# Kernel tuning notes

Measured on AMD Instinct MI355X. Metric: run time of the kernel, lower is better.

Reference implementation:

```python
import jax, jax.numpy as jnp
import numpy as np

N, E, D, H = 50000, 800000, 128, 8
DH = D // H  # 16
EPS_LN = 1e-5


def layer_norm(x, gamma, beta):
    mu = jnp.mean(x, axis=-1, keepdims=True)
    var = jnp.var(x, axis=-1, keepdims=True)
    return (x - mu) * jax.lax.rsqrt(var + EPS_LN) * gamma + beta


def setup_inputs() -> dict:
    key = jax.random.key(0)
    ks = jax.random.split(key, 12)
    s = 1.0 / np.sqrt(D)
    x = jax.random.normal(ks[0], (N, D), dtype=jnp.float32)
    src = jax.random.randint(ks[1], (E,), 0, N, dtype=jnp.int32)
    dst = jax.random.randint(ks[2], (E,), 0, N, dtype=jnp.int32)
    Wq = jax.random.normal(ks[3], (D, D), dtype=jnp.float32) * s
    Wk = jax.random.normal(ks[4], (D, D), dtype=jnp.float32) * s
    Wv = jax.random.normal(ks[5], (D, D), dtype=jnp.float32) * s
    Wo = jax.random.normal(ks[6], (D, D), dtype=jnp.float32) * s
    bq = jnp.zeros((D,), jnp.float32)
    bk = jnp.zeros((D,), jnp.float32)
    bv = jnp.zeros((D,), jnp.float32)
    bo = jnp.zeros((D,), jnp.float32)
    gamma1 = jnp.ones((D,), jnp.float32)
    beta1 = jnp.zeros((D,), jnp.float32)
    gamma2 = jnp.ones((D,), jnp.float32)
    beta2 = jnp.zeros((D,), jnp.float32)
    return dict(x=x, src=src, dst=dst, Wq=Wq, bq=bq, Wk=Wk, bk=bk, Wv=Wv, bv=bv,
                Wo=Wo, bo=bo, gamma1=gamma1, beta1=beta1, gamma2=gamma2, beta2=beta2)


def reference(x, src, dst, Wq, bq, Wk, bk, Wv, bv, Wo, bo, gamma1, beta1, gamma2, beta2):
    n = x.shape[0]
    Q = (x @ Wq + bq).reshape(n, H, DH)   # [N,H,Dh]
    K = (x @ Wk + bk).reshape(n, H, DH)
    V = (x @ Wv + bv).reshape(n, H, DH)
    # edge-wise QK dot: score[e,h] = sum_d K[src[e],h,d] * Q[dst[e],h,d]
    score = jnp.sum(K[src] * Q[dst], axis=-1) / np.sqrt(DH)  # [E,H]
    score = jnp.exp(jnp.clip(score, -5.0, 5.0))
    # scatter-sum weighted values and normalizer over destination nodes
    wV = jax.ops.segment_sum(V[src] * score[..., None], dst, num_segments=n)  # [N,H,Dh]
    z = jax.ops.segment_sum(score, dst, num_segments=n)                        # [N,H]
    attn = (wV / (z[..., None] + 1e-3)).reshape(n, D)
    h = layer_norm(x + attn, gamma1, beta1)
    # sublayer: h + relu(O(LN(h)))  (dropout = 0)
    h = h + jax.nn.relu(layer_norm(h, gamma2, beta2) @ Wo + bo)
    return h
```

## Files before the change

### kernel.cpp

```cpp
#include <hip/hip_runtime.h>

typedef unsigned short ushort_t;
typedef __attribute__((ext_vector_type(8))) short short8;
typedef __attribute__((ext_vector_type(4))) float floatx4;
typedef __attribute__((ext_vector_type(2))) _Float16 half2v;
typedef __attribute__((ext_vector_type(8))) _Float16 half8;

#define QSCALE 0.36067376022224085f
#define SCLIP  7.2134752044448170f

__device__ __forceinline__ unsigned h2u(half2v h) {
    union { half2v h; unsigned u; } x; x.h = h; return x.u;
}
__device__ __forceinline__ half2v u2h(unsigned u) {
    union { unsigned u; half2v h; } x; x.u = u; return x.h;
}
__device__ __forceinline__ ushort_t h2us(_Float16 h) {
    union { _Float16 h; ushort_t u; } x; x.h = h; return x.u;
}
__device__ __forceinline__ unsigned pkrtz(float a, float b) {
    auto h = __builtin_amdgcn_cvt_pkrtz(a, b);
    union { decltype(h) h2; unsigned u; } x; x.h2 = h; return x.u;
}
__device__ __forceinline__ float dot2h(half2v a, half2v b, float c) {
#if __has_builtin(__builtin_amdgcn_fdot2)
    return __builtin_amdgcn_fdot2(a, b, c, false);
#else
    return c + (float)a[0] * (float)b[0] + (float)a[1] * (float)b[1];
#endif
}
__device__ __forceinline__ half2v pk_shfl_add(half2v a, int m) {
    unsigned o = (unsigned)__shfl_xor((int)h2u(a), m, 64);
    return a + u2h(o);
}

__global__ __launch_bounds__(256) void transpose_swz(
    const float* __restrict__ Wq, const float* __restrict__ Wk,
    const float* __restrict__ Wv, const float* __restrict__ Wo,
    ushort_t* __restrict__ out, int* __restrict__ deg, int N)
{
    int flat = (blockIdx.y * gridDim.x + blockIdx.x) * 256 + threadIdx.x;
    for (int i = flat; i < N; i += 8192) deg[i] = 0;

    const float* W = (blockIdx.y == 0) ? Wq : (blockIdx.y == 1) ? Wk :
                     (blockIdx.y == 2) ? Wv : Wo;
    ushort_t* T = out + (size_t)blockIdx.y * 128 * 128;
    int t = blockIdx.x * 256 + threadIdx.x;
    int kg = t >> 7;
    int n  = t & 127;
    int k0 = kg * 8;
    float w[8];
    #pragma unroll
    for (int j = 0; j < 8; j++)
        w[j] = W[(size_t)(k0 + j) * 128 + n];
    int4 o;
    o.x = (int)pkrtz(w[0], w[1]);
    o.y = (int)pkrtz(w[2], w[3]);
    o.z = (int)pkrtz(w[4], w[5]);
    o.w = (int)pkrtz(w[6], w[7]);
    int sn = n >> 4, l15 = n & 15, kb = kg >> 2, quad = kg & 3;
    size_t f = ((size_t)((sn * 4 + kb) * 4 + quad)) * 128 + (size_t)l15 * 8;
    *(int4*)(T + f) = o;
}

__global__ __launch_bounds__(256) void gemm_qkv(
    const float* __restrict__ X, const ushort_t* __restrict__ Wsw,
    const float* __restrict__ bq, const float* __restrict__ bk, const float* __restrict__ bv,
    ushort_t* __restrict__ Q, ushort_t* __restrict__ KV, int M,
    const int* __restrict__ dst, int* __restrict__ deg, int E)
{
    __shared__ ushort_t Xs[64 * 136];
    int tid = threadIdx.x;
    int rowBase = blockIdx.x * 64;
    int wsel = blockIdx.y;
    const ushort_t* Wmat = Wsw + (size_t)wsel * 128 * 128;
    const float* bias = (wsel == 0) ? bq : (wsel == 1) ? bk : bv;

    {
        int nblk = gridDim.x * gridDim.y;
        int fb = blockIdx.y * gridDim.x + blockIdx.x;
        int per = (E + nblk - 1) / nblk;
        int end = min(per * (fb + 1), E);
        for (int i = per * fb + tid; i < end; i += 256)
            atomicAdd(&deg[dst[i]], 1);
    }

    int r = tid >> 4;
    int c = (tid & 15) * 8;
    for (int rr = 0; rr < 64; rr += 16) {
        int row = rowBase + rr + r;
        int rc = (row < M) ? row : (M - 1);
        const float* p = X + (size_t)rc * 128 + c;
        float4 f0 = *(const float4*)p;
        float4 f1 = *(const float4*)(p + 4);
        int4 pv;
        pv.x = (int)pkrtz(f0.x, f0.y);
        pv.y = (int)pkrtz(f0.z, f0.w);
        pv.z = (int)pkrtz(f1.x, f1.y);
        pv.w = (int)pkrtz(f1.z, f1.w);
        *(int4*)&Xs[(rr + r) * 136 + c] = pv;
    }
    __syncthreads();

    int lane = tid & 63, wave = tid >> 6;
    int wm = wave * 16;
    int l15 = lane & 15, quad = lane >> 4;
    floatx4 acc[8] = {};
    for (int kb = 0; kb < 4; kb++) {
        half8 a = *(const half8*)&Xs[(wm + l15) * 136 + kb * 32 + quad * 8];
        for (int sn = 0; sn < 8; sn++) {
            half8 b = *(const half8*)(Wmat + (size_t)(sn * 4 + kb) * 512 + lane * 8);
            acc[sn] = __builtin_amdgcn_mfma_f32_16x16x32_f16(a, b, acc[sn], 0, 0, 0);
        }
    }

    float scl = (wsel == 0) ? QSCALE : 1.0f;
    for (int sn = 0; sn < 8; sn++) {
        int col = sn * 16 + l15;
        float bia = bias[col];
        for (int rr2 = 0; rr2 < 4; rr2++) {
            int rl = wm + quad * 4 + rr2;
            Xs[rl * 136 + col] = h2us((_Float16)((acc[sn][rr2] + bia) * scl));
        }
    }
    for (int it = 0; it < 4; it++) {
        int idx = it * 64 + lane;
        int rl = idx >> 4;
        int seg = idx & 15;
        int row = rowBase + wm + rl;
        if (row < M) {
            short8 v = *(const short8*)&Xs[(wm + rl) * 136 + seg * 8];
            if (wsel == 0) {
                *(short8*)(Q + (size_t)row * 128 + seg * 8) = v;
            } else {
                *(short8*)(KV + (size_t)row * 256 + seg * 16 + ((wsel == 2) ? 8 : 0)) = v;
            }
        }
    }
}

__global__ __launch_bounds__(256) void k_scan_blocks(const int* __restrict__ deg, int* __restrict__ offs,
                                                     int* __restrict__ bsums, int n) {
    __shared__ int s[256];
    int i = blockIdx.x * 256 + threadIdx.x;
    int v = (i < n) ? deg[i] : 0;
    s[threadIdx.x] = v;
    __syncthreads();
    for (int d = 1; d < 256; d <<= 1) {
        int t = (threadIdx.x >= d) ? s[threadIdx.x - d] : 0;
        __syncthreads();
        s[threadIdx.x] += t;
        __syncthreads();
    }
    int incl = s[threadIdx.x];
    if (i < n) offs[i] = incl - v;
    if (threadIdx.x == 255) bsums[blockIdx.x] = incl;
}

__global__ __launch_bounds__(256) void k_add_base(int* __restrict__ offs, int* __restrict__ cursor,
                                                  const int* __restrict__ bs, int nb, int n, int E) {
    int tid = threadIdx.x;
    int acc = 0;
    for (int t = tid; t < nb; t += 256)
        if (t < (int)blockIdx.x) acc += bs[t];
    for (int m = 1; m < 64; m <<= 1) acc += __shfl_xor(acc, m, 64);
    __shared__ int sw[4];
    if ((tid & 63) == 0) sw[tid >> 6] = acc;
    __syncthreads();
    int base = sw[0] + sw[1] + sw[2] + sw[3];
    int i = blockIdx.x * 256 + tid;
    if (i < n) {
        int o = offs[i] + base;
        offs[i] = o;
        cursor[i] = o;
    }
    if (blockIdx.x == 0 && tid == 0) offs[n] = E;
}

__global__ __launch_bounds__(256) void k_scatter(const int* __restrict__ src, const int* __restrict__ dst,
                                                 int* __restrict__ cursor, int* __restrict__ eadj, int E) {
    int i = blockIdx.x * 256 + threadIdx.x;
    if (i < E) {
        int p = atomicAdd(&cursor[dst[i]], 1);
        eadj[p] = src[i];
    }
}

__global__ __launch_bounds__(256) void edge_attn(
    const ushort_t* __restrict__ Qb, const ushort_t* __restrict__ KV,
    const float* __restrict__ xin,
    const int* __restrict__ offs, const int* __restrict__ eadj,
    const float* __restrict__ g1, const float* __restrict__ be1,
    const float* __restrict__ g2, const float* __restrict__ be2,
    ushort_t* __restrict__ h1out, ushort_t* __restrict__ ln2out, int N)
{
    int wave = threadIdx.x >> 6, lane = threadIdx.x & 63;
    int n = blockIdx.x * 4 + wave;
    if (n >= N) return;
    int l15 = lane & 15, grp = lane >> 4;

    uint4 qp = *(const uint4*)(Qb + (size_t)n * 128 + l15 * 8);
    half2v q0 = u2h(qp.x), q1 = u2h(qp.y), q2 = u2h(qp.z), q3 = u2h(qp.w);

    int s0 = offs[n], s1 = offs[n + 1];
    half2v a01 = u2h(0u), a23 = u2h(0u), a45 = u2h(0u), a67 = u2h(0u);
    float z = 0.f;
    for (int base = s0; base < s1; base += 64) {
        int cnt = min(s1 - base, 64);
        int ee = (base + lane < s1) ? eadj[base + lane] : 0;
        #pragma unroll 2
        for (int j = 0; j < cnt; j += 4) {
            int jj = j + grp;
            int sn = __shfl(ee, jj, 64);
            const ushort_t* kvp = KV + (size_t)sn * 256 + l15 * 16;
            uint4 kk = *(const uint4*)kvp;
            uint4 vv = *(const uint4*)(kvp + 8);
            float d = dot2h(u2h(kk.x), q0,
                      dot2h(u2h(kk.y), q1,
                      dot2h(u2h(kk.z), q2,
                      dot2h(u2h(kk.w), q3, 0.f))));
            d += __shfl_xor(d, 1, 64);
            float sc = fminf(SCLIP, fmaxf(-SCLIP, d));
            float e = (jj < cnt) ? exp2f(sc) : 0.f;
            _Float16 eh = (_Float16)e;
            half2v ep; ep[0] = eh; ep[1] = eh;
            a01 += u2h(vv.x) * ep;
            a23 += u2h(vv.y) * ep;
            a45 += u2h(vv.z) * ep;
            a67 += u2h(vv.w) * ep;
            z += e;
        }
    }
    a01 = pk_shfl_add(a01, 16); a01 = pk_shfl_add(a01, 32);
    a23 = pk_shfl_add(a23, 16); a23 = pk_shfl_add(a23, 32);
    a45 = pk_shfl_add(a45, 16); a45 = pk_shfl_add(a45, 32);
    a67 = pk_shfl_add(a67, 16); a67 = pk_shfl_add(a67, 32);
    z += __shfl_xor(z, 16, 64); z += __shfl_xor(z, 32, 64);
    float inv = 1.f / (z + 1e-3f);

    half2v ap = (grp == 0) ? a01 : (grp == 1) ? a23 : (grp == 2) ? a45 : a67;
    int col = l15 * 8 + grp * 2;
    float a0 = (float)ap[0], a1 = (float)ap[1];

    float2 xv = *(const float2*)(xin + (size_t)n * 128 + col);
    float t0 = fmaf(a0, inv, xv.x);
    float t1 = fmaf(a1, inv, xv.y);

    float s = t0 + t1, s2 = t0 * t0 + t1 * t1;
    #pragma unroll
    for (int m = 1; m < 64; m <<= 1) { s += __shfl_xor(s, m, 64); s2 += __shfl_xor(s2, m, 64); }
    float mu = s * (1.f / 128.f);
    float var = s2 * (1.f / 128.f) - mu * mu;
    float rstd = rsqrtf(var + 1e-5f);

    float2 gv = *(const float2*)(g1 + col);
    float2 bv = *(const float2*)(be1 + col);
    float h0 = (t0 - mu) * rstd * gv.x + bv.x;
    float h1 = (t1 - mu) * rstd * gv.y + bv.y;
    *(unsigned*)(h1out + (size_t)n * 128 + col) = pkrtz(h0, h1);

    s = h0 + h1; s2 = h0 * h0 + h1 * h1;
    #pragma unroll
    for (int m = 1; m < 64; m <<= 1) { s += __shfl_xor(s, m, 64); s2 += __shfl_xor(s2, m, 64); }
    float mu2 = s * (1.f / 128.f);
    float var2 = s2 * (1.f / 128.f) - mu2 * mu2;
    float rstd2 = rsqrtf(var2 + 1e-5f);

    float2 g2v = *(const float2*)(g2 + col);
    float2 b2v = *(const float2*)(be2 + col);
    float l0 = (h0 - mu2) * rstd2 * g2v.x + b2v.x;
    float l1 = (h1 - mu2) * rstd2 * g2v.y + b2v.y;
    *(unsigned*)(ln2out + (size_t)n * 128 + col) = pkrtz(l0, l1);
}

__global__ __launch_bounds__(256) void gemm_o(
    const ushort_t* __restrict__ X, const ushort_t* __restrict__ Wsw,
    const float* __restrict__ bo, const ushort_t* __restrict__ h1in,
    float* __restrict__ Out, int M)
{
    __shared__ ushort_t As[64 * 136];
    int tid = threadIdx.x;
    int rowBase = blockIdx.x * 64;
    int snBase = blockIdx.y * 4;
    int colBase = snBase * 16;

    int r = tid >> 4;
    int c = (tid & 15) * 8;
    for (int rr = 0; rr < 64; rr += 16) {
        int row = rowBase + rr + r;
        int rc = (row < M) ? row : (M - 1);
        short8 v = *(const short8*)(X + (size_t)rc * 128 + c);
        *(short8*)&As[(rr + r) * 136 + c] = v;
    }
    __syncthreads();

    int lane = tid & 63, wave = tid >> 6;
    int wm = wave * 16;
    int l15 = lane & 15, quad = lane >> 4;
    floatx4 acc[4] = {};
    for (int kb = 0; kb < 4; kb++) {
        half8 a = *(const half8*)&As[(wm + l15) * 136 + kb * 32 + quad * 8];
        for (int s = 0; s < 4; s++) {
            half8 b = *(const half8*)(Wsw + (size_t)((snBase + s) * 4 + kb) * 512 + lane * 8);
            acc[s] = __builtin_amdgcn_mfma_f32_16x16x32_f16(a, b, acc[s], 0, 0, 0);
        }
    }

    float* Cs = (float*)As;
    for (int s = 0; s < 4; s++) {
        int cl = s * 16 + l15;
        float bia = bo[colBase + cl];
        for (int rr2 = 0; rr2 < 4; rr2++) {
            int rl = wm + quad * 4 + rr2;
            Cs[rl * 68 + cl] = fmaxf(acc[s][rr2] + bia, 0.f);
        }
    }
    for (int it = 0; it < 4; it++) {
        int idx = it * 64 + lane;
        int rl = idx >> 4;
        int c4 = (idx & 15) * 4;
        int row = rowBase + wm + rl;
        if (row < M) {
            float4 v = *(const float4*)&Cs[(wm + rl) * 68 + c4];
            uint2 hp = *(const uint2*)(h1in + (size_t)row * 128 + colBase + c4);
            half2v ha = u2h(hp.x), hb = u2h(hp.y);
            v.x += (float)ha[0];
            v.y += (float)ha[1];
            v.z += (float)hb[0];
            v.w += (float)hb[1];
            *(float4*)(Out + (size_t)row * 128 + colBase + c4) = v;
        }
    }
}

extern "C" void kernel_launch(void* const* d_in, const int* in_sizes, int n_in,
                              void* d_out, int out_size, void* d_ws, size_t ws_size,
                              hipStream_t stream) {
    const int D = 128;
    const int N = in_sizes[0] / D;
    const int E = in_sizes[1];

    const float* x   = (const float*)d_in[0];
    const int*   src = (const int*)d_in[1];
    const int*   dst = (const int*)d_in[2];
    const float* Wq  = (const float*)d_in[3];
    const float* bq  = (const float*)d_in[4];
    const float* Wk  = (const float*)d_in[5];
    const float* bk  = (const float*)d_in[6];
    const float* Wv  = (const float*)d_in[7];
    const float* bv  = (const float*)d_in[8];
    const float* Wo  = (const float*)d_in[9];
    const float* bo  = (const float*)d_in[10];
    const float* g1  = (const float*)d_in[11];
    const float* be1 = (const float*)d_in[12];
    const float* g2  = (const float*)d_in[13];
    const float* be2 = (const float*)d_in[14];

    char* ws = (char*)d_ws;
    size_t o = 0;
    auto alloc = [&](size_t b) { o = (o + 255) & ~(size_t)255; size_t r = o; o += b; return r; };
    ushort_t* Qb   = (ushort_t*)(ws + alloc((size_t)N * D * 2));
    ushort_t* KVb  = (ushort_t*)(ws + alloc((size_t)N * D * 4));
    ushort_t* ln2  = (ushort_t*)(ws + alloc((size_t)N * D * 2));
    ushort_t* h1   = (ushort_t*)(ws + alloc((size_t)N * D * 2));
    ushort_t* Wt   = (ushort_t*)(ws + alloc((size_t)4 * 128 * 128 * 2));
    int*      deg  = (int*)(ws + alloc((size_t)N * 4));
    int*      offs = (int*)(ws + alloc((size_t)(N + 1) * 4));
    int*      cur  = (int*)(ws + alloc((size_t)N * 4));
    int*      bsum = (int*)(ws + alloc((size_t)256 * 4));
    int*      eadj = (int*)(ws + alloc((size_t)E * 4));

    int nScanBlocks = (N + 255) / 256;
    int nEdgeBlocks = (E + 255) / 256;
    int nRowTiles = (N + 63) / 64;

    transpose_swz<<<dim3(8, 4), 256, 0, stream>>>(Wq, Wk, Wv, Wo, Wt, deg, N);
    gemm_qkv<<<dim3(nRowTiles, 3), 256, 0, stream>>>(x, Wt, bq, bk, bv, Qb, KVb, N, dst, deg, E);
    k_scan_blocks<<<nScanBlocks, 256, 0, stream>>>(deg, offs, bsum, N);
    k_add_base<<<nScanBlocks, 256, 0, stream>>>(offs, cur, bsum, nScanBlocks, N, E);
    k_scatter<<<nEdgeBlocks, 256, 0, stream>>>(src, dst, cur, eadj, E);
    edge_attn<<<(N + 3) / 4, 256, 0, stream>>>(Qb, KVb, x, offs, eadj, g1, be1, g2, be2, h1, ln2, N);
    gemm_o<<<dim3(nRowTiles, 2), 256, 0, stream>>>(ln2, Wt + 3 * 128 * 128, bo, h1, (float*)d_out, N);
}
```

Measured before the change: 267.7 us.

## Reuse loaded X tile across Q/K/V and output columns; batch edge gathers

The QKV GEMM now has each block compute all three projections from a single staged X tile, instead of launching three blocks that each reload and convert X. Likewise the output GEMM computes all 128 columns per block rather than splitting columns across two blocks. In the edge attention loop, four KV gathers are issued before any compute to raise memory-level parallelism. In exchange, grids are smaller with more registers and shared memory per block, which may lower occupancy, and the edge loop now does more redundant masked work on the tail.

```diff
diff --git a/kernel.cpp b/kernel.cpp
--- a/kernel.cpp
+++ b/kernel.cpp
@@ -70,15 +70,13 @@
     const int* __restrict__ dst, int* __restrict__ deg, int E)
 {
     __shared__ ushort_t Xs[64 * 136];
+    __shared__ ushort_t Cs[64 * 136];
     int tid = threadIdx.x;
     int rowBase = blockIdx.x * 64;
-    int wsel = blockIdx.y;
-    const ushort_t* Wmat = Wsw + (size_t)wsel * 128 * 128;
-    const float* bias = (wsel == 0) ? bq : (wsel == 1) ? bk : bv;
 
     {
-        int nblk = gridDim.x * gridDim.y;
-        int fb = blockIdx.y * gridDim.x + blockIdx.x;
+        int nblk = gridDim.x;
+        int fb = blockIdx.x;
         int per = (E + nblk - 1) / nblk;
         int end = min(per * (fb + 1), E);
         for (int i = per * fb + tid; i < end; i += 256)
@@ -105,35 +103,41 @@
     int lane = tid & 63, wave = tid >> 6;
     int wm = wave * 16;
     int l15 = lane & 15, quad = lane >> 4;
-    floatx4 acc[8] = {};
-    for (int kb = 0; kb < 4; kb++) {
-        half8 a = *(const half8*)&Xs[(wm + l15) * 136 + kb * 32 + quad * 8];
+
+    for (int wsel = 0; wsel < 3; wsel++) {
+        const ushort_t* Wmat = Wsw + (size_t)wsel * 128 * 128;
+        const float* bias = (wsel == 0) ? bq : (wsel == 1) ? bk : bv;
+
+        floatx4 acc[8] = {};
+        for (int kb = 0; kb < 4; kb++) {
+            half8 a = *(const half8*)&Xs[(wm + l15) * 136 + kb * 32 + quad * 8];
+            for (int sn = 0; sn < 8; sn++) {
+                half8 b = *(const half8*)(Wmat + (size_t)(sn * 4 + kb) * 512 + lane * 8);
+                acc[sn] = __builtin_amdgcn_mfma_f32_16x16x32_f16(a, b, acc[sn], 0, 0, 0);
+            }
+        }
+
+        float scl = (wsel == 0) ? QSCALE : 1.0f;
         for (int sn = 0; sn < 8; sn++) {
-            half8 b = *(const half8*)(Wmat + (size_t)(sn * 4 + kb) * 512 + lane * 8);
-            acc[sn] = __builtin_amdgcn_mfma_f32_16x16x32_f16(a, b, acc[sn], 0, 0, 0);
-        }
-    }
-
-    float scl = (wsel == 0) ? QSCALE : 1.0f;
-    for (int sn = 0; sn < 8; sn++) {
-        int col = sn * 16 + l15;
-        float bia = bias[col];
-        for (int rr2 = 0; rr2 < 4; rr2++) {
-            int rl = wm + quad * 4 + rr2;
-            Xs[rl * 136 + col] = h2us((_Float16)((acc[sn][rr2] + bia) * scl));
-        }
-    }
-    for (int it = 0; it < 4; it++) {
-        int idx = it * 64 + lane;
-        int rl = idx >> 4;
-        int seg = idx & 15;
-        int row = rowBase + wm + rl;
-        if (row < M) {
-            short8 v = *(const short8*)&Xs[(wm + rl) * 136 + seg * 8];
-            if (wsel == 0) {
-                *(short8*)(Q + (size_t)row * 128 + seg * 8) = v;
-            } else {
-                *(short8*)(KV + (size_t)row * 256 + seg * 16 + ((wsel == 2) ? 8 : 0)) = v;
+            int col = sn * 16 + l15;
+            float bia = bias[col];
+            for (int rr2 = 0; rr2 < 4; rr2++) {
+                int rl = wm + quad * 4 + rr2;
+                Cs[rl * 136 + col] = h2us((_Float16)((acc[sn][rr2] + bia) * scl));
+            }
+        }
+        for (int it = 0; it < 4; it++) {
+            int idx = it * 64 + lane;
+            int rl = idx >> 4;
+            int seg = idx & 15;
+            int row = rowBase + wm + rl;
+            if (row < M) {
+                short8 v = *(const short8*)&Cs[(wm + rl) * 136 + seg * 8];
+                if (wsel == 0) {
+                    *(short8*)(Q + (size_t)row * 128 + seg * 8) = v;
+                } else {
+                    *(short8*)(KV + (size_t)row * 256 + seg * 16 + ((wsel == 2) ? 8 : 0)) = v;
+                }
             }
         }
     }
@@ -208,13 +212,8 @@
     for (int base = s0; base < s1; base += 64) {
         int cnt = min(s1 - base, 64);
         int ee = (base + lane < s1) ? eadj[base + lane] : 0;
-        #pragma unroll 2
-        for (int j = 0; j < cnt; j += 4) {
-            int jj = j + grp;
-            int sn = __shfl(ee, jj, 64);
-            const ushort_t* kvp = KV + (size_t)sn * 256 + l15 * 16;
-            uint4 kk = *(const uint4*)kvp;
-            uint4 vv = *(const uint4*)(kvp + 8);
+
+        auto comp = [&](uint4 kk, uint4 vv, int jj) {
             float d = dot2h(u2h(kk.x), q0,
                       dot2h(u2h(kk.y), q1,
                       dot2h(u2h(kk.z), q2,
@@ -229,6 +228,26 @@
             a45 += u2h(vv.z) * ep;
             a67 += u2h(vv.w) * ep;
             z += e;
+        };
+
+        for (int j0 = 0; j0 < cnt; j0 += 16) {
+            int t0 = j0 + grp;
+            int sn0 = __shfl(ee, t0, 64);
+            int sn1 = __shfl(ee, t0 + 4, 64);
+            int sn2 = __shfl(ee, t0 + 8, 64);
+            int sn3 = __shfl(ee, t0 + 12, 64);
+            const ushort_t* p0 = KV + (size_t)sn0 * 256 + l15 * 16;
+            const ushort_t* p1 = KV + (size_t)sn1 * 256 + l15 * 16;
+            const ushort_t* p2 = KV + (size_t)sn2 * 256 + l15 * 16;
+            const ushort_t* p3 = KV + (size_t)sn3 * 256 + l15 * 16;
+            uint4 kk0 = *(const uint4*)p0, vv0 = *(const uint4*)(p0 + 8);
+            uint4 kk1 = *(const uint4*)p1, vv1 = *(const uint4*)(p1 + 8);
+            uint4 kk2 = *(const uint4*)p2, vv2 = *(const uint4*)(p2 + 8);
+            uint4 kk3 = *(const uint4*)p3, vv3 = *(const uint4*)(p3 + 8);
+            comp(kk0, vv0, t0);
+            comp(kk1, vv1, t0 + 4);
+            comp(kk2, vv2, t0 + 8);
+            comp(kk3, vv3, t0 + 12);
         }
     }
     a01 = pk_shfl_add(a01, 16); a01 = pk_shfl_add(a01, 32);
@@ -279,10 +298,9 @@
     float* __restrict__ Out, int M)
 {
     __shared__ ushort_t As[64 * 136];
+    __shared__ float Cs[64 * 68];
     int tid = threadIdx.x;
     int rowBase = blockIdx.x * 64;
-    int snBase = blockIdx.y * 4;
-    int colBase = snBase * 16;
 
     int r = tid >> 4;
     int c = (tid & 15) * 8;
@@ -297,38 +315,41 @@
     int lane = tid & 63, wave = tid >> 6;
     int wm = wave * 16;
     int l15 = lane & 15, quad = lane >> 4;
-    floatx4 acc[4] = {};
+    floatx4 acc[8] = {};
     for (int kb = 0; kb < 4; kb++) {
         half8 a = *(const half8*)&As[(wm + l15) * 136 + kb * 32 + quad * 8];
+        for (int sn = 0; sn < 8; sn++) {
+            half8 b = *(const half8*)(Wsw + (size_t)(sn * 4 + kb) * 512 + lane * 8);
+            acc[sn] = __builtin_amdgcn_mfma_f32_16x16x32_f16(a, b, acc[sn], 0, 0, 0);
+        }
+    }
+
+    for (int half = 0; half < 2; half++) {
+        int snB = half * 4;
+        int colBase = half * 64;
         for (int s = 0; s < 4; s++) {
-            half8 b = *(const half8*)(Wsw + (size_t)((snBase + s) * 4 + kb) * 512 + lane * 8);
-            acc[s] = __builtin_amdgcn_mfma_f32_16x16x32_f16(a, b, acc[s], 0, 0, 0);
-        }
-    }
-
-    float* Cs = (float*)As;
-    for (int s = 0; s < 4; s++) {
-        int cl = s * 16 + l15;
-        float bia = bo[colBase + cl];
-        for (int rr2 = 0; rr2 < 4; rr2++) {
-            int rl = wm + quad * 4 + rr2;
-            Cs[rl * 68 + cl] = fmaxf(acc[s][rr2] + bia, 0.f);
-        }
-    }
-    for (int it = 0; it < 4; it++) {
-        int idx = it * 64 + lane;
-        int rl = idx >> 4;
-        int c4 = (idx & 15) * 4;
-        int row = rowBase + wm + rl;
-        if (row < M) {
-            float4 v = *(const float4*)&Cs[(wm + rl) * 68 + c4];
-            uint2 hp = *(const uint2*)(h1in + (size_t)row * 128 + colBase + c4);
-            half2v ha = u2h(hp.x), hb = u2h(hp.y);
-            v.x += (float)ha[0];
-            v.y += (float)ha[1];
-            v.z += (float)hb[0];
-            v.w += (float)hb[1];
-            *(float4*)(Out + (size_t)row * 128 + colBase + c4) = v;
+            int cl = s * 16 + l15;
+            float bia = bo[colBase + cl];
+            for (int rr2 = 0; rr2 < 4; rr2++) {
+                int rl = wm + quad * 4 + rr2;
+                Cs[rl * 68 + cl] = fmaxf(acc[snB + s][rr2] + bia, 0.f);
+            }
+        }
+        for (int it = 0; it < 4; it++) {
+            int idx = it * 64 + lane;
+            int rl = idx >> 4;
+            int c4 = (idx & 15) * 4;
+            int row = rowBase + wm + rl;
+            if (row < M) {
+                float4 v = *(const float4*)&Cs[(wm + rl) * 68 + c4];
+                uint2 hp = *(const uint2*)(h1in + (size_t)row * 128 + colBase + c4);
+                half2v ha = u2h(hp.x), hb = u2h(hp.y);
+                v.x += (float)ha[0];
+                v.y += (float)ha[1];
+                v.z += (float)hb[0];
+                v.w += (float)hb[1];
+                *(float4*)(Out + (size_t)row * 128 + colBase + c4) = v;
+            }
         }
     }
 }
@@ -375,10 +396,10 @@
     int nRowTiles = (N + 63) / 64;
 
     transpose_swz<<<dim3(8, 4), 256, 0, stream>>>(Wq, Wk, Wv, Wo, Wt, deg, N);
-    gemm_qkv<<<dim3(nRowTiles, 3), 256, 0, stream>>>(x, Wt, bq, bk, bv, Qb, KVb, N, dst, deg, E);
+    gemm_qkv<<<nRowTiles, 256, 0, stream>>>(x, Wt, bq, bk, bv, Qb, KVb, N, dst, deg, E);
     k_scan_blocks<<<nScanBlocks, 256, 0, stream>>>(deg, offs, bsum, N);
     k_add_base<<<nScanBlocks, 256, 0, stream>>>(offs, cur, bsum, nScanBlocks, N, E);
     k_scatter<<<nEdgeBlocks, 256, 0, stream>>>(src, dst, cur, eadj, E);
     edge_attn<<<(N + 3) / 4, 256, 0, stream>>>(Qb, KVb, x, offs, eadj, g1, be1, g2, be2, h1, ln2, N);
-    gemm_o<<<dim3(nRowTiles, 2), 256, 0, stream>>>(ln2, Wt + 3 * 128 * 128, bo, h1, (float*)d_out, N);
-}
+    gemm_o<<<nRowTiles, 256, 0, stream>>>(ln2, Wt + 3 * 128 * 128, bo, h1, (float*)d_out, N);
+}
```

Result: slower. 277.8 us (+3.8%).
